# Performance work log

Hardware: AMD Instinct MI355X
Metric: run time of the kernel (lower is better)

## Reference

```python
import jax, jax.numpy as jnp
import numpy as np
from jax import lax

NQ = 4      # num_qubits
DEPTH = 2
DIM = 2 ** NQ  # 16

def _maxpool2(x):
    # MaxPool2d(kernel_size=2, stride=1), NCHW
    return lax.reduce_window(x, -jnp.inf, lax.max, (1, 1, 2, 2), (1, 1, 1, 1), 'VALID')

def _conv(x, w, b, stride, pad):
    y = lax.conv_general_dilated(x, w, (stride, stride), [(pad, pad), (pad, pad)],
                                 dimension_numbers=('NCHW', 'OIHW', 'NCHW'))
    return y + b[None, :, None, None]

def _apply_1q(state, gate, q):
    # state: (B, 16) complex64; gate: (2,2) shared or (B,2,2) per-sample. wire 0 = MSB.
    B = state.shape[0]
    s = state.reshape(B, 2 ** q, 2, 2 ** (NQ - 1 - q))
    sub = 'ij,bljr->blir' if gate.ndim == 2 else 'bij,bljr->blir'
    return jnp.einsum(sub, gate, s).reshape(B, DIM)

def _quantum_head(angles, weights):
    # Batched statevector simulation of: RX(angles[i]) encoding, then DEPTH x
    # [RY(w) on every wire, CZ chain], then <Z_0>, <Z_1>.
    B = angles.shape[0]
    state = jnp.zeros((B, DIM), jnp.complex64).at[:, 0].set(1.0)
    for q in range(NQ):  # RX encoding (per-sample angles)
        t = angles[:, q] * 0.5
        c = jnp.cos(t).astype(jnp.complex64)
        s = (-1j) * jnp.sin(t).astype(jnp.complex64)
        gate = jnp.stack([jnp.stack([c, s], -1), jnp.stack([s, c], -1)], -2)  # (B,2,2)
        state = _apply_1q(state, gate, q)
    idxs = jnp.arange(DIM)
    w_idx = 0
    for _ in range(DEPTH):
        for q in range(NQ):  # RY(weights) shared across batch
            t = weights[w_idx] * 0.5
            w_idx += 1
            c, s = jnp.cos(t), jnp.sin(t)
            gate = jnp.stack([jnp.stack([c, -s]), jnp.stack([s, c])]).astype(jnp.complex64)
            state = _apply_1q(state, gate, q)
        for q in range(NQ - 1):  # CZ(q, q+1): -1 phase where both bits set
            both = ((idxs >> (NQ - 1 - q)) & 1) & ((idxs >> (NQ - 2 - q)) & 1)
            phase = jnp.where(both == 1, -1.0, 1.0).astype(jnp.complex64)
            state = state * phase[None, :]
    probs = state.real ** 2 + state.imag ** 2  # (B,16) float32
    logits = []
    for q in range(2):  # expval PauliZ on wires 0,1
        sign = 1.0 - 2.0 * ((idxs >> (NQ - 1 - q)) & 1).astype(jnp.float32)
        logits.append(probs @ sign)
    return jnp.stack(logits, -1)  # (B,2)


def setup_inputs() -> dict:
    key = jax.random.key(0)
    ks = jax.random.split(key, 12)
    x = jax.random.normal(ks[0], (256, 3, 250, 250), jnp.float32)
    w1 = jax.random.normal(ks[1], (6, 3, 5, 5), jnp.float32) * 0.05
    b1 = jnp.zeros((6,), jnp.float32)
    w2 = jax.random.normal(ks[2], (15, 6, 3, 3), jnp.float32) * 0.05
    b2 = jnp.zeros((15,), jnp.float32)
    fc1_w = jax.random.normal(ks[3], (120, 55815), jnp.float32) * 0.004
    fc1_b = jnp.zeros((120,), jnp.float32)
    fc2_w = jax.random.normal(ks[4], (84, 120), jnp.float32) * 0.09
    fc2_b = jnp.zeros((84,), jnp.float32)
    fc3_w = jax.random.normal(ks[5], (4, 84), jnp.float32) * 0.1
    fc3_b = jnp.zeros((4,), jnp.float32)
    qweights = jax.random.normal(ks[6], (NQ * DEPTH,), jnp.float32)
    return {'x': x, 'w1': w1, 'b1': b1, 'w2': w2, 'b2': b2,
            'fc1_w': fc1_w, 'fc1_b': fc1_b, 'fc2_w': fc2_w, 'fc2_b': fc2_b,
            'fc3_w': fc3_w, 'fc3_b': fc3_b, 'qweights': qweights}


def reference(x, w1, b1, w2, b2, fc1_w, fc1_b, fc2_w, fc2_b, fc3_w, fc3_b, qweights):
    # Dropout layers act as identity (eval mode).
    h = jax.nn.relu(_conv(x, w1, b1, stride=2, pad=1))   # (B,6,124,124)
    h = _maxpool2(h)                                      # (B,6,123,123)
    h = jax.nn.relu(_conv(h, w2, b2, stride=2, pad=1))   # (B,15,62,62)
    h = _maxpool2(h)                                      # (B,15,61,61)
    h = h.reshape(h.shape[0], -1)                         # (B,55815)
    h = jax.nn.relu(h @ fc1_w.T + fc1_b)
    h = jax.nn.relu(h @ fc2_w.T + fc2_b)
    angles = h @ fc3_w.T + fc3_b                          # (B,4)
    logits = _quantum_head(angles, qweights)              # (B,2)
    return jax.nn.softmax(logits, axis=-1)
```

## Files before the change

kernel.cpp:

```cpp
#include <hip/hip_runtime.h>
#include <hip/hip_bf16.h>
#include <math.h>

#define B 256
#define FC1_K   55815
#define FC1_N   120
#define FC2_N   84
#define KP        57344
#define FC1_SPLIT 128
#define FC1_KC    (KP / FC1_SPLIT)

typedef __attribute__((ext_vector_type(8))) short bf16x8;
typedef __attribute__((ext_vector_type(4))) float f32x4;

static __device__ __forceinline__ unsigned short bf16_bits(float f) {
    __hip_bfloat16 h = __float2bfloat16(f);
    return *(unsigned short*)&h;
}

#define ASYNC_CP(g, l) __builtin_amdgcn_global_load_lds( \
    (const __attribute__((address_space(1))) void*)(g),  \
    (__attribute__((address_space(3))) void*)(l), 4, 0, 0)

__global__ __launch_bounds__(256) void prep_kernel(
    const float* __restrict__ w1, const float* __restrict__ w2,
    const float* __restrict__ fc1_w,
    float* __restrict__ w1p, float* __restrict__ w2p,
    float* __restrict__ zeros, unsigned short* __restrict__ wb) {
    const int n = blockIdx.y;
    const int k = blockIdx.x * 256 + threadIdx.x;
    unsigned short v = 0;
    if (n < FC1_N && k < FC1_K) v = bf16_bits(fc1_w[(size_t)n * FC1_K + k]);
    wb[(size_t)n * KP + k] = v;

    if (blockIdx.x == 0 && n == 0) {
        int t = threadIdx.x;
        for (int f = t; f < 450; f += 256) {
            int o = f % 6, tap = f / 6;
            int kx = tap % 5, r2 = tap / 5, ky = r2 % 5, c = r2 / 5;
            w1p[f] = w1[(o * 3 + c) * 25 + ky * 5 + kx];
        }
        for (int f = t; f < 810; f += 256) {
            int o = f % 15, tap = f / 15;
            int kx = tap % 3, r2 = tap / 3, ky = r2 % 3, c = r2 / 3;
            w2p[f] = w2[(o * 6 + c) * 9 + ky * 3 + kx];
        }
        if (t < 64) zeros[t] = 0.f;
    }
}

__global__ __launch_bounds__(256) void conv1_pool1_kernel(
    const float* __restrict__ x, const float* __restrict__ w1p,
    const float* __restrict__ b1, unsigned short* __restrict__ pool1,
    const float* __restrict__ zeros) {
    __shared__ __align__(16) float in_t[19 * 256 + 8];
    __shared__ __align__(16) unsigned short out_t[6 * 8 * 132];

    const int tid = threadIdx.x;
    const int wave = tid >> 6, lane = tid & 63;
    const int PB = 7 * blockIdx.x;
    const int b  = blockIdx.y;
    const int cg = tid & 31, rr = tid >> 5;
    const int iyb = 2 * PB - 1;

    float acc[4][6];
    #pragma unroll
    for (int j = 0; j < 4; ++j)
        #pragma unroll
        for (int o = 0; o < 6; ++o) acc[j][o] = b1[o];

    for (int c = 0; c < 3; ++c) {
        __syncthreads();
        const float* xp = x + (size_t)(b * 3 + c) * 62500;
        #pragma unroll
        for (int i = 0; i < 19; ++i) {
            int chunk = wave * 19 + i;
            int f = chunk * 64 + lane;
            int row = f >> 8, m = f & 255;
            int iy = iyb + row, col = m - 1;
            const float* g = ((unsigned)iy < 250u && (unsigned)col < 250u)
                             ? (xp + iy * 250 + col) : zeros;
            ASYNC_CP(g, &in_t[chunk * 64]);
        }
        __syncthreads();
        const float* wc = w1p + c * 150;
        #pragma unroll
        for (int ky = 0; ky < 5; ++ky) {
            const float* rp = &in_t[(2 * rr + ky) * 256 + 8 * cg];
            float f[12];
            float4 v0 = *(const float4*)rp;
            float4 v1 = *(const float4*)(rp + 4);
            float4 v2 = *(const float4*)(rp + 8);
            f[0]=v0.x; f[1]=v0.y; f[2]=v0.z; f[3]=v0.w;
            f[4]=v1.x; f[5]=v1.y; f[6]=v1.z; f[7]=v1.w;
            f[8]=v2.x; f[9]=v2.y; f[10]=v2.z; f[11]=v2.w;
            #pragma unroll
            for (int kx = 0; kx < 5; ++kx) {
                const float* wp = wc + (ky * 5 + kx) * 6;
                #pragma unroll
                for (int j = 0; j < 4; ++j) {
                    float xv = f[2 * j + kx];
                    #pragma unroll
                    for (int o = 0; o < 6; ++o) acc[j][o] += xv * wp[o];
                }
            }
        }
    }
    #pragma unroll
    for (int o = 0; o < 6; ++o) {
        unsigned short h0 = bf16_bits(fmaxf(acc[0][o], 0.f));
        unsigned short h1 = bf16_bits(fmaxf(acc[1][o], 0.f));
        unsigned short h2 = bf16_bits(fmaxf(acc[2][o], 0.f));
        unsigned short h3 = bf16_bits(fmaxf(acc[3][o], 0.f));
        uint2 pk;
        pk.x = (unsigned)h0 | ((unsigned)h1 << 16);
        pk.y = (unsigned)h2 | ((unsigned)h3 << 16);
        *(uint2*)&out_t[(o * 8 + rr) * 132 + 4 * cg] = pk;
    }
    __syncthreads();
    for (int it = tid; it < 6 * 7 * 32; it += 256) {
        int g = it & 31, rem = it >> 5;
        int pyl = rem % 7, oc = rem / 7;
        int py = PB + pyl;
        if (py >= 123) continue;
        const unsigned short* q0 = &out_t[(oc * 8 + pyl) * 132 + 4 * g];
        const unsigned short* q1 = q0 + 132;
        uint2 ua = *(const uint2*)q0;
        uint2 ub = *(const uint2*)q1;
        unsigned short va[5] = {(unsigned short)(ua.x & 0xffff), (unsigned short)(ua.x >> 16),
                                (unsigned short)(ua.y & 0xffff), (unsigned short)(ua.y >> 16), q0[4]};
        unsigned short vb[5] = {(unsigned short)(ub.x & 0xffff), (unsigned short)(ub.x >> 16),
                                (unsigned short)(ub.y & 0xffff), (unsigned short)(ub.y >> 16), q1[4]};
        unsigned short* dst = pool1 + ((size_t)(b * 6 + oc) * 123 + py) * 128;
        #pragma unroll
        for (int j = 0; j < 4; ++j) {
            int px = 4 * g + j;
            if (px >= 127) continue;
            unsigned short m = 0;
            if (px <= 122) {
                unsigned short m0 = va[j] > va[j+1] ? va[j] : va[j+1];
                unsigned short m1 = vb[j] > vb[j+1] ? vb[j] : vb[j+1];
                m = m0 > m1 ? m0 : m1;
            }
            dst[1 + px] = m;
        }
        if (g == 0) dst[0] = 0;
    }
}

__global__ __launch_bounds__(128) void conv2_pool2_kernel(
    const unsigned short* __restrict__ pool1, const float* __restrict__ w2p,
    const float* __restrict__ b2, unsigned short* __restrict__ A,
    const unsigned int* __restrict__ zerosu) {
    __shared__ __align__(16) unsigned int in2[17 * 64 + 4];
    __shared__ __align__(16) unsigned short out2[15 * 8 * 68];

    const int tid = threadIdx.x;
    const int wave = tid >> 6, lane = tid & 63;
    const int PB = 7 * blockIdx.x;
    const int b  = blockIdx.y;
    const int cg = tid & 15, rr = tid >> 4;
    const int iyb = 2 * PB - 1;

    float acc[4][15];
    #pragma unroll
    for (int j = 0; j < 4; ++j)
        #pragma unroll
        for (int o = 0; o < 15; ++o) acc[j][o] = b2[o];

    const unsigned int* p1u = (const unsigned int*)pool1;
    for (int c = 0; c < 6; ++c) {
        __syncthreads();
        const unsigned int* pp = p1u + (size_t)(b * 6 + c) * (123 * 64);
        #pragma unroll
        for (int i = 0; i < 9; ++i) {
            int chunk = wave * 9 + i;
            if (chunk < 17) {
                int f = chunk * 64 + lane;
                int row = f >> 6, off = f & 63;
                int iy = iyb + row;
                const unsigned int* g = ((unsigned)iy < 123u)
                                        ? (pp + iy * 64 + off) : zerosu;
                ASYNC_CP(g, &in2[chunk * 64]);
            }
        }
        __syncthreads();
        #pragma unroll
        for (int ky = 0; ky < 3; ++ky) {
            const unsigned int* rp = &in2[(2 * rr + ky) * 64 + 4 * cg];
            uint4 u4 = *(const uint4*)rp;
            unsigned int u5 = rp[4];
            float f[10];
            f[0] = __uint_as_float(u4.x << 16); f[1] = __uint_as_float(u4.x & 0xffff0000u);
            f[2] = __uint_as_float(u4.y << 16); f[3] = __uint_as_float(u4.y & 0xffff0000u);
            f[4] = __uint_as_float(u4.z << 16); f[5] = __uint_as_float(u4.z & 0xffff0000u);
            f[6] = __uint_as_float(u4.w << 16); f[7] = __uint_as_float(u4.w & 0xffff0000u);
            f[8] = __uint_as_float(u5  << 16);  f[9] = __uint_as_float(u5  & 0xffff0000u);
            #pragma unroll
            for (int kx = 0; kx < 3; ++kx) {
                const float* wp = w2p + (c * 9 + ky * 3 + kx) * 15;
                #pragma unroll
                for (int j = 0; j < 4; ++j) {
                    float xv = f[2 * j + kx];
                    #pragma unroll
                    for (int o = 0; o < 15; ++o) acc[j][o] += xv * wp[o];
                }
            }
        }
    }
    #pragma unroll
    for (int o = 0; o < 15; ++o) {
        unsigned short h0 = bf16_bits(fmaxf(acc[0][o], 0.f));
        unsigned short h1 = bf16_bits(fmaxf(acc[1][o], 0.f));
        unsigned short h2 = bf16_bits(fmaxf(acc[2][o], 0.f));
        unsigned short h3 = bf16_bits(fmaxf(acc[3][o], 0.f));
        uint2 pk;
        pk.x = (unsigned)h0 | ((unsigned)h1 << 16);
        pk.y = (unsigned)h2 | ((unsigned)h3 << 16);
        *(uint2*)&out2[(o * 8 + rr) * 68 + 4 * cg] = pk;
    }
    __syncthreads();
    for (int it = tid; it < 15 * 7 * 16; it += 128) {
        int g = it & 15, rem = it >> 4;
        int pyl = rem % 7, oc = rem / 7;
        int py = PB + pyl;
        if (py >= 61) continue;
        const unsigned short* q0 = &out2[(oc * 8 + pyl) * 68 + 4 * g];
        const unsigned short* q1 = q0 + 68;
        uint2 ua = *(const uint2*)q0;
        uint2 ub = *(const uint2*)q1;
        unsigned short va[5] = {(unsigned short)(ua.x & 0xffff), (unsigned short)(ua.x >> 16),
                                (unsigned short)(ua.y & 0xffff), (unsigned short)(ua.y >> 16), q0[4]};
        unsigned short vb[5] = {(unsigned short)(ub.x & 0xffff), (unsigned short)(ub.x >> 16),
                                (unsigned short)(ub.y & 0xffff), (unsigned short)(ub.y >> 16), q1[4]};
        #pragma unroll
        for (int j = 0; j < 4; ++j) {
            int px = 4 * g + j;
            if (px < 61) {
                unsigned short m0 = va[j] > va[j+1] ? va[j] : va[j+1];
                unsigned short m1 = vb[j] > vb[j+1] ? vb[j] : vb[j+1];
                unsigned short m = m0 > m1 ? m0 : m1;
                A[(size_t)b * KP + (oc * 61 + py) * 61 + px] = m;
            }
        }
    }
}

__global__ __launch_bounds__(256) void fc1_mfma_kernel(
    const __hip_bfloat16* __restrict__ A, const __hip_bfloat16* __restrict__ W,
    float* __restrict__ partial) {
    const int wave = threadIdx.x >> 6, lane = threadIdx.x & 63;
    const int mrow = lane & 15, quad = lane >> 4;
    const int m0 = blockIdx.x * 128 + wave * 32;
    const int k0 = blockIdx.y * FC1_KC;

    f32x4 acc[2][8];
    #pragma unroll
    for (int i = 0; i < 2; ++i)
        #pragma unroll
        for (int j = 0; j < 8; ++j) acc[i][j] = (f32x4){0.f, 0.f, 0.f, 0.f};

    const short* Ap = (const short*)A;
    const short* Wp = (const short*)W;
    for (int ks = 0; ks < FC1_KC; ks += 32) {
        const int kk = k0 + ks + quad * 8;
        const bf16x8 a0 = *(const bf16x8*)(Ap + (size_t)(m0 + mrow) * KP + kk);
        const bf16x8 a1 = *(const bf16x8*)(Ap + (size_t)(m0 + 16 + mrow) * KP + kk);
        #pragma unroll
        for (int nt = 0; nt < 8; ++nt) {
            const bf16x8 bb = *(const bf16x8*)(Wp + (size_t)(nt * 16 + mrow) * KP + kk);
            acc[0][nt] = __builtin_amdgcn_mfma_f32_16x16x32_bf16(a0, bb, acc[0][nt], 0, 0, 0);
            acc[1][nt] = __builtin_amdgcn_mfma_f32_16x16x32_bf16(a1, bb, acc[1][nt], 0, 0, 0);
        }
    }
    float* po = partial + (size_t)blockIdx.y * (256 * 128);
    #pragma unroll
    for (int mt = 0; mt < 2; ++mt)
        #pragma unroll
        for (int nt = 0; nt < 8; ++nt)
            #pragma unroll
            for (int r = 0; r < 4; ++r)
                po[(m0 + mt * 16 + quad * 4 + r) * 128 + nt * 16 + mrow] = acc[mt][nt][r];
}

__global__ __launch_bounds__(256) void tail_kernel(
    const float* __restrict__ partial, const float* __restrict__ fc1_b,
    const float* __restrict__ fc2_w, const float* __restrict__ fc2_b,
    const float* __restrict__ fc3_w, const float* __restrict__ fc3_b,
    const float* __restrict__ qw, float* __restrict__ out) {
    __shared__ float h1p[2][FC1_N];
    __shared__ float h1[FC1_N];
    __shared__ float h2[FC2_N];
    __shared__ float ang[4];
    int b = blockIdx.x;
    int t = threadIdx.x;
    int grp = t >> 7, tt = t & 127;

    if (tt < FC1_N) {
        const float* p = partial + b * 128 + tt;
        float sum = 0.f;
        #pragma unroll 4
        for (int s = grp * 64; s < grp * 64 + 64; ++s) sum += p[(size_t)s * (256 * 128)];
        h1p[grp][tt] = sum;
    }
    __syncthreads();
    if (t < FC1_N) h1[t] = fmaxf(h1p[0][t] + h1p[1][t] + fc1_b[t], 0.f);
    __syncthreads();
    if (t < FC2_N) {
        float acc = fc2_b[t];
        const float* w = fc2_w + t * FC1_N;
        for (int k = 0; k < FC1_N; ++k) acc += h1[k] * w[k];
        h2[t] = fmaxf(acc, 0.f);
    }
    __syncthreads();
    if (t < 4) {
        float acc = fc3_b[t];
        const float* w = fc3_w + t * FC2_N;
        for (int k = 0; k < FC2_N; ++k) acc += h2[k] * w[k];
        ang[t] = acc;
    }
    __syncthreads();
    if (t == 0) {
        float sr[16], si[16];
        #pragma unroll
        for (int i = 0; i < 16; ++i) { sr[i] = 0.f; si[i] = 0.f; }
        sr[0] = 1.f;
        for (int q = 0; q < 4; ++q) {
            float th = ang[q] * 0.5f;
            float c = cosf(th), s = sinf(th);
            int mask = 1 << (3 - q);
            #pragma unroll
            for (int i = 0; i < 16; ++i) {
                if (i & mask) continue;
                int i1 = i | mask;
                float a0r = sr[i], a0i = si[i], a1r = sr[i1], a1i = si[i1];
                sr[i]  = c * a0r + s * a1i;
                si[i]  = c * a0i - s * a1r;
                sr[i1] = c * a1r + s * a0i;
                si[i1] = c * a1i - s * a0r;
            }
        }
        int widx = 0;
        for (int d = 0; d < 2; ++d) {
            for (int q = 0; q < 4; ++q) {
                float th = qw[widx++] * 0.5f;
                float c = cosf(th), s = sinf(th);
                int mask = 1 << (3 - q);
                #pragma unroll
                for (int i = 0; i < 16; ++i) {
                    if (i & mask) continue;
                    int i1 = i | mask;
                    float a0r = sr[i], a0i = si[i], a1r = sr[i1], a1i = si[i1];
                    sr[i]  = c * a0r - s * a1r;
                    si[i]  = c * a0i - s * a1i;
                    sr[i1] = s * a0r + c * a1r;
                    si[i1] = s * a0i + c * a1i;
                }
            }
            for (int q = 0; q < 3; ++q) {
                int m1 = 1 << (3 - q), m2 = 1 << (2 - q);
                #pragma unroll
                for (int i = 0; i < 16; ++i) {
                    if ((i & m1) && (i & m2)) { sr[i] = -sr[i]; si[i] = -si[i]; }
                }
            }
        }
        float l0 = 0.f, l1 = 0.f;
        #pragma unroll
        for (int i = 0; i < 16; ++i) {
            float p = sr[i] * sr[i] + si[i] * si[i];
            l0 += (i & 8) ? -p : p;
            l1 += (i & 4) ? -p : p;
        }
        float m = fmaxf(l0, l1);
        float e0 = expf(l0 - m), e1 = expf(l1 - m);
        float inv = 1.f / (e0 + e1);
        out[b * 2 + 0] = e0 * inv;
        out[b * 2 + 1] = e1 * inv;
    }
}

extern "C" void kernel_launch(void* const* d_in, const int* in_sizes, int n_in,
                              void* d_out, int out_size, void* d_ws, size_t ws_size,
                              hipStream_t stream) {
    const float* x     = (const float*)d_in[0];
    const float* w1    = (const float*)d_in[1];
    const float* b1    = (const float*)d_in[2];
    const float* w2    = (const float*)d_in[3];
    const float* b2    = (const float*)d_in[4];
    const float* fc1_w = (const float*)d_in[5];
    const float* fc1_b = (const float*)d_in[6];
    const float* fc2_w = (const float*)d_in[7];
    const float* fc2_b = (const float*)d_in[8];
    const float* fc3_w = (const float*)d_in[9];
    const float* fc3_b = (const float*)d_in[10];
    const float* qw    = (const float*)d_in[11];
    float* out = (float*)d_out;

    char* ws = (char*)d_ws;
    const size_t O_POOL1  = 0;
    const size_t O_A      = O_POOL1 + 48365568;
    const size_t O_W      = O_A + 29360128;
    const size_t O_PART   = O_W + 14680064;
    const size_t O_W1P    = O_PART + 16777216;
    const size_t O_W2P    = O_W1P + 2048;
    const size_t O_ZERO   = O_W2P + 4096;
    unsigned short* pool1   = (unsigned short*)(ws + O_POOL1);
    __hip_bfloat16* A_bf16  = (__hip_bfloat16*)(ws + O_A);
    __hip_bfloat16* W_bf16  = (__hip_bfloat16*)(ws + O_W);
    float*          partial = (float*)(ws + O_PART);
    float*          w1p     = (float*)(ws + O_W1P);
    float*          w2p     = (float*)(ws + O_W2P);
    float*          zeros   = (float*)(ws + O_ZERO);

    prep_kernel<<<dim3(KP / 256, 128), 256, 0, stream>>>(
        w1, w2, fc1_w, w1p, w2p, zeros, (unsigned short*)W_bf16);
    conv1_pool1_kernel<<<dim3(18, B), 256, 0, stream>>>(x, w1p, b1, pool1, zeros);
    conv2_pool2_kernel<<<dim3(9, B), 128, 0, stream>>>(pool1, w2p, b2,
                                                       (unsigned short*)A_bf16,
                                                       (const unsigned int*)zeros);
    fc1_mfma_kernel<<<dim3(2, FC1_SPLIT), 256, 0, stream>>>(A_bf16, W_bf16, partial);
    tail_kernel<<<B, 256, 0, stream>>>(partial, fc1_b, fc2_w, fc2_b,
                                       fc3_w, fc3_b, qw, out);
}
```

Baseline: 441.7 us.

## Double fc1 split-K, vectorize weight prep, parallelize quantum sim across lanes

Raises the fc1 split-K factor from 128 to 256 so the MFMA GEMM launches more blocks, and grows the partial buffer and the tail reduction to match (4 groups of 64 slices, 512 threads). The fc1 weight bf16 conversion now handles 8 elements per thread and writes them with one vector store. The 16-amplitude statevector simulation moves from one thread to 16 lanes that exchange amplitudes with xor shuffles and use fast sin/cos intrinsics. The cost is twice the partial-sum traffic into the tail kernel, plus slightly less accurate trig.

Measured after the change: 421.4 us. 4.6% less time.

```diff
diff --git a/kernel.cpp b/kernel.cpp
--- a/kernel.cpp
+++ b/kernel.cpp
@@ -7,7 +7,7 @@
 #define FC1_N   120
 #define FC2_N   84
 #define KP        57344
-#define FC1_SPLIT 128
+#define FC1_SPLIT 256
 #define FC1_KC    (KP / FC1_SPLIT)
 
 typedef __attribute__((ext_vector_type(8))) short bf16x8;
@@ -28,10 +28,22 @@
     float* __restrict__ w1p, float* __restrict__ w2p,
     float* __restrict__ zeros, unsigned short* __restrict__ wb) {
     const int n = blockIdx.y;
-    const int k = blockIdx.x * 256 + threadIdx.x;
-    unsigned short v = 0;
-    if (n < FC1_N && k < FC1_K) v = bf16_bits(fc1_w[(size_t)n * FC1_K + k]);
-    wb[(size_t)n * KP + k] = v;
+    const int k0 = blockIdx.x * 2048 + threadIdx.x * 8;
+    bf16x8 v8;
+    #pragma unroll
+    for (int i = 0; i < 8; ++i) v8[i] = 0;
+    if (n < FC1_N) {
+        const float* src = fc1_w + (size_t)n * FC1_K + k0;
+        if (k0 + 8 <= FC1_K) {
+            #pragma unroll
+            for (int i = 0; i < 8; ++i) v8[i] = (short)bf16_bits(src[i]);
+        } else {
+            #pragma unroll
+            for (int i = 0; i < 8; ++i)
+                if (k0 + i < FC1_K) v8[i] = (short)bf16_bits(src[i]);
+        }
+    }
+    *(bf16x8*)(wb + (size_t)n * KP + k0) = v8;
 
     if (blockIdx.x == 0 && n == 0) {
         int t = threadIdx.x;
@@ -283,12 +295,12 @@
                 po[(m0 + mt * 16 + quad * 4 + r) * 128 + nt * 16 + mrow] = acc[mt][nt][r];
 }
 
-__global__ __launch_bounds__(256) void tail_kernel(
+__global__ __launch_bounds__(512) void tail_kernel(
     const float* __restrict__ partial, const float* __restrict__ fc1_b,
     const float* __restrict__ fc2_w, const float* __restrict__ fc2_b,
     const float* __restrict__ fc3_w, const float* __restrict__ fc3_b,
     const float* __restrict__ qw, float* __restrict__ out) {
-    __shared__ float h1p[2][FC1_N];
+    __shared__ float h1p[4][FC1_N];
     __shared__ float h1[FC1_N];
     __shared__ float h2[FC2_N];
     __shared__ float ang[4];
@@ -299,12 +311,13 @@
     if (tt < FC1_N) {
         const float* p = partial + b * 128 + tt;
         float sum = 0.f;
-        #pragma unroll 4
+        #pragma unroll 8
         for (int s = grp * 64; s < grp * 64 + 64; ++s) sum += p[(size_t)s * (256 * 128)];
         h1p[grp][tt] = sum;
     }
     __syncthreads();
-    if (t < FC1_N) h1[t] = fmaxf(h1p[0][t] + h1p[1][t] + fc1_b[t], 0.f);
+    if (t < FC1_N)
+        h1[t] = fmaxf(h1p[0][t] + h1p[1][t] + h1p[2][t] + h1p[3][t] + fc1_b[t], 0.f);
     __syncthreads();
     if (t < FC2_N) {
         float acc = fc2_b[t];
@@ -320,63 +333,55 @@
         ang[t] = acc;
     }
     __syncthreads();
-    if (t == 0) {
-        float sr[16], si[16];
-        #pragma unroll
-        for (int i = 0; i < 16; ++i) { sr[i] = 0.f; si[i] = 0.f; }
-        sr[0] = 1.f;
+    if (t < 16) {
+        const int lane = t;
+        float sr = (lane == 0) ? 1.f : 0.f, si = 0.f;
+        #pragma unroll
         for (int q = 0; q < 4; ++q) {
             float th = ang[q] * 0.5f;
-            float c = cosf(th), s = sinf(th);
-            int mask = 1 << (3 - q);
-            #pragma unroll
-            for (int i = 0; i < 16; ++i) {
-                if (i & mask) continue;
-                int i1 = i | mask;
-                float a0r = sr[i], a0i = si[i], a1r = sr[i1], a1i = si[i1];
-                sr[i]  = c * a0r + s * a1i;
-                si[i]  = c * a0i - s * a1r;
-                sr[i1] = c * a1r + s * a0i;
-                si[i1] = c * a1i - s * a0r;
-            }
+            float c = __cosf(th), s = __sinf(th);
+            int mask = 8 >> q;
+            float pr = __shfl_xor(sr, mask, 16);
+            float pi = __shfl_xor(si, mask, 16);
+            float nr = c * sr + s * pi;
+            float ni = c * si - s * pr;
+            sr = nr; si = ni;
         }
         int widx = 0;
+        #pragma unroll
         for (int d = 0; d < 2; ++d) {
+            #pragma unroll
             for (int q = 0; q < 4; ++q) {
                 float th = qw[widx++] * 0.5f;
-                float c = cosf(th), s = sinf(th);
-                int mask = 1 << (3 - q);
-                #pragma unroll
-                for (int i = 0; i < 16; ++i) {
-                    if (i & mask) continue;
-                    int i1 = i | mask;
-                    float a0r = sr[i], a0i = si[i], a1r = sr[i1], a1i = si[i1];
-                    sr[i]  = c * a0r - s * a1r;
-                    si[i]  = c * a0i - s * a1i;
-                    sr[i1] = s * a0r + c * a1r;
-                    si[i1] = s * a0i + c * a1i;
-                }
-            }
+                float c = __cosf(th), s = __sinf(th);
+                int mask = 8 >> q;
+                float pr = __shfl_xor(sr, mask, 16);
+                float pi = __shfl_xor(si, mask, 16);
+                float sg = (lane & mask) ? s : -s;
+                sr = c * sr + sg * pr;
+                si = c * si + sg * pi;
+            }
+            #pragma unroll
             for (int q = 0; q < 3; ++q) {
-                int m1 = 1 << (3 - q), m2 = 1 << (2 - q);
-                #pragma unroll
-                for (int i = 0; i < 16; ++i) {
-                    if ((i & m1) && (i & m2)) { sr[i] = -sr[i]; si[i] = -si[i]; }
-                }
-            }
-        }
-        float l0 = 0.f, l1 = 0.f;
-        #pragma unroll
-        for (int i = 0; i < 16; ++i) {
-            float p = sr[i] * sr[i] + si[i] * si[i];
-            l0 += (i & 8) ? -p : p;
-            l1 += (i & 4) ? -p : p;
-        }
-        float m = fmaxf(l0, l1);
-        float e0 = expf(l0 - m), e1 = expf(l1 - m);
-        float inv = 1.f / (e0 + e1);
-        out[b * 2 + 0] = e0 * inv;
-        out[b * 2 + 1] = e1 * inv;
+                int m1 = 8 >> q, m2 = 4 >> q;
+                if ((lane & m1) && (lane & m2)) { sr = -sr; si = -si; }
+            }
+        }
+        float p = sr * sr + si * si;
+        float v0 = (lane & 8) ? -p : p;
+        float v1 = (lane & 4) ? -p : p;
+        #pragma unroll
+        for (int off = 8; off >= 1; off >>= 1) {
+            v0 += __shfl_xor(v0, off, 16);
+            v1 += __shfl_xor(v1, off, 16);
+        }
+        if (lane == 0) {
+            float m = fmaxf(v0, v1);
+            float e0 = expf(v0 - m), e1 = expf(v1 - m);
+            float inv = 1.f / (e0 + e1);
+            out[b * 2 + 0] = e0 * inv;
+            out[b * 2 + 1] = e1 * inv;
+        }
     }
 }
 
@@ -402,7 +407,7 @@
     const size_t O_A      = O_POOL1 + 48365568;
     const size_t O_W      = O_A + 29360128;
     const size_t O_PART   = O_W + 14680064;
-    const size_t O_W1P    = O_PART + 16777216;
+    const size_t O_W1P    = O_PART + 33554432;
     const size_t O_W2P    = O_W1P + 2048;
     const size_t O_ZERO   = O_W2P + 4096;
     unsigned short* pool1   = (unsigned short*)(ws + O_POOL1);
@@ -413,13 +418,13 @@
     float*          w2p     = (float*)(ws + O_W2P);
     float*          zeros   = (float*)(ws + O_ZERO);
 
-    prep_kernel<<<dim3(KP / 256, 128), 256, 0, stream>>>(
+    prep_kernel<<<dim3(KP / 2048, 128), 256, 0, stream>>>(
         w1, w2, fc1_w, w1p, w2p, zeros, (unsigned short*)W_bf16);
     conv1_pool1_kernel<<<dim3(18, B), 256, 0, stream>>>(x, w1p, b1, pool1, zeros);
     conv2_pool2_kernel<<<dim3(9, B), 128, 0, stream>>>(pool1, w2p, b2,
                                                        (unsigned short*)A_bf16,
                                                        (const unsigned int*)zeros);
     fc1_mfma_kernel<<<dim3(2, FC1_SPLIT), 256, 0, stream>>>(A_bf16, W_bf16, partial);
-    tail_kernel<<<B, 256, 0, stream>>>(partial, fc1_b, fc2_w, fc2_b,
+    tail_kernel<<<B, 512, 0, stream>>>(partial, fc1_b, fc2_w, fc2_b,
                                        fc3_w, fc3_b, qw, out);
 }
```
